# Performance work log

Hardware: AMD Instinct MI355X
Metric: run time of the kernel (lower is better)

## Reference

```python
import jax, jax.numpy as jnp
import numpy as np

N, C = 8192, 64

def setup_inputs() -> dict:
    key = jax.random.key(0)
    kA, kY = jax.random.split(key)
    A = jax.random.uniform(kA, (N, N), dtype=jnp.float32)
    Y = jax.random.normal(kY, (N, C), dtype=jnp.float32)
    return {"A": A, "Y": Y}

def reference(A, Y):
    # soft assignments
    Ys = jax.nn.softmax(Y, axis=1)                 # [n, C]
    # M[i, j] = Y_i^T A Y_j  (C x C); diag == total_ewc, strict-upper == pairwise ice
    M = jnp.einsum('ni,nm,mj->ij', Ys, A, Ys)      # two GEMMs, no n x n x C tensor
    total_ewc = jnp.diag(M)                        # [C]
    nwc = Ys.sum(axis=0)                           # [C]
    max_ewc = (nwc * (nwc - 1.0) + 1e-08) / 2.0
    cohesion = (total_ewc / max_ewc).sum()
    inter_cluster_edges = jnp.sum(jnp.triu(M, 1))  # sum_{i<j} Y_i^T A Y_j
    total_edges = A.sum()
    coupling = inter_cluster_edges / (total_edges + 1e-09)
    return -cohesion + coupling
```

## Files before the change

### kernel.cpp

```cpp
#include <hip/hip_runtime.h>
#include <hip/hip_bf16.h>

#define NN 8192
#define CC 64
#define KSPLIT 8
#define KCHUNK (NN / KSPLIT)
#define BK 64
#define NSTEPS (KCHUNK / BK)

typedef __bf16 bf16;
typedef __bf16 bf16x8 __attribute__((ext_vector_type(8)));
typedef float f32x4 __attribute__((ext_vector_type(4)));
typedef unsigned short us8 __attribute__((ext_vector_type(8)));

__global__ __launch_bounds__(256) void k1_softmax(const float* __restrict__ Yin,
                                                  float* __restrict__ Ys,
                                                  unsigned short* __restrict__ YsT,
                                                  float* __restrict__ nwc_part) {
    __shared__ float lds_t[64][65];
    __shared__ float nwc_lds[4][64];
    const int t = threadIdx.x;
    const int w = t >> 6, lane = t & 63;
    const int b = blockIdx.x;
    const int r0 = b * 64;
    float nwc_acc = 0.f;
    for (int it = 0; it < 16; ++it) {
        const int rl = it * 4 + w;
        const int row = r0 + rl;
        float y = Yin[row * CC + lane];
        float mx = y;
        #pragma unroll
        for (int m = 32; m >= 1; m >>= 1) mx = fmaxf(mx, __shfl_xor(mx, m, 64));
        float e = __expf(y - mx);
        float s = e;
        #pragma unroll
        for (int m = 32; m >= 1; m >>= 1) s += __shfl_xor(s, m, 64);
        float ys = e / s;
        Ys[row * CC + lane] = ys;
        lds_t[lane][rl] = ys;
        nwc_acc += ys;
    }
    nwc_lds[w][lane] = nwc_acc;
    __syncthreads();
    if (t < 64)
        nwc_part[b * 64 + t] = nwc_lds[0][t] + nwc_lds[1][t] + nwc_lds[2][t] + nwc_lds[3][t];
    const int c = t >> 2, q = t & 3;
    unsigned short tmp[16];
    #pragma unroll
    for (int i = 0; i < 16; ++i) {
        float v = lds_t[c][q * 16 + i];
        tmp[i] = __builtin_bit_cast(unsigned short, (__bf16)v);
    }
    us8* dst = (us8*)(&YsT[(size_t)c * NN + r0 + q * 16]);
    dst[0] = *(us8*)(&tmp[0]);
    dst[1] = *(us8*)(&tmp[8]);
}

__global__ __launch_bounds__(256) void k2_gemm(const float* __restrict__ A,
                                               const unsigned short* __restrict__ YsT,
                                               float* __restrict__ Bpart,
                                               float* __restrict__ edges_part) {
    __shared__ __align__(16) float ldsA[64 * 64];
    __shared__ __align__(16) unsigned short ldsB[64 * 64];
    __shared__ float ered[4];
    const int t = threadIdx.x;
    const int w = t >> 6, lane = t & 63;
    const int rb = blockIdx.x;
    const int kb = blockIdx.y;
    const int row0 = rb * 64;
    const int k0 = kb * KCHUNK;
    const int lq = lane >> 4;
    const int l15 = lane & 15;

    const int ar  = lane >> 4;
    const int ach = lane & 15;
    const int bc  = lane >> 3;
    const int bch = lane & 7;

    float esum = 0.f;
    f32x4 acc[4] = {};

    for (int s = 0; s < NSTEPS; ++s) {
        const int kbase = k0 + s * BK;
        __syncthreads();
        #pragma unroll
        for (int p = 0; p < 16; ++p) {
            const int r = p * 4 + ar;
            const float* src = A + (size_t)(row0 + r) * NN + kbase + ((ach ^ (r & 7)) << 2);
            __builtin_amdgcn_global_load_lds(
                (const __attribute__((address_space(1))) unsigned int*)src,
                (__attribute__((address_space(3))) unsigned int*)&ldsA[p * 256], 16, 0, 0);
        }
        #pragma unroll
        for (int q = 0; q < 8; ++q) {
            const int c = q * 8 + bc;
            const unsigned short* src = YsT + (size_t)c * NN + kbase + ((bch ^ (c & 7)) << 3);
            __builtin_amdgcn_global_load_lds(
                (const __attribute__((address_space(1))) unsigned int*)src,
                (__attribute__((address_space(3))) unsigned int*)&ldsB[q * 512], 16, 0, 0);
        }
        __syncthreads();
        #pragma unroll
        for (int kk = 0; kk < 2; ++kk) {
            const int r = w * 16 + l15;
            const int cc = kk * 8 + lq * 2;
            const int ch0 = cc ^ (r & 7);
            const f32x4 fa0 = *(const f32x4*)&ldsA[r * 64 + (ch0 << 2)];
            const f32x4 fa1 = *(const f32x4*)&ldsA[r * 64 + ((ch0 ^ 1) << 2)];
            esum += (fa0[0] + fa0[1] + fa0[2] + fa0[3]) + (fa1[0] + fa1[1] + fa1[2] + fa1[3]);
            bf16x8 a;
            a[0] = (__bf16)fa0[0]; a[1] = (__bf16)fa0[1]; a[2] = (__bf16)fa0[2]; a[3] = (__bf16)fa0[3];
            a[4] = (__bf16)fa1[0]; a[5] = (__bf16)fa1[1]; a[6] = (__bf16)fa1[2]; a[7] = (__bf16)fa1[3];
            #pragma unroll
            for (int t4 = 0; t4 < 4; ++t4) {
                const int col = t4 * 16 + l15;
                const int chB = (kk * 4 + lq) ^ (col & 7);
                const bf16x8 bb = *(const bf16x8*)&ldsB[col * 64 + (chB << 3)];
                acc[t4] = __builtin_amdgcn_mfma_f32_16x16x32_bf16(a, bb, acc[t4], 0, 0, 0);
            }
        }
    }

    const size_t base = ((size_t)kb * NN + row0) * CC;
    #pragma unroll
    for (int t4 = 0; t4 < 4; ++t4) {
        const int col = t4 * 16 + l15;
        #pragma unroll
        for (int r = 0; r < 4; ++r) {
            const int grow = w * 16 + lq * 4 + r;
            Bpart[base + (size_t)grow * CC + col] = acc[t4][r];
        }
    }
    #pragma unroll
    for (int m = 32; m >= 1; m >>= 1) esum += __shfl_xor(esum, m, 64);
    if (lane == 0) ered[w] = esum;
    __syncthreads();
    if (t == 0) edges_part[rb * KSPLIT + kb] = ered[0] + ered[1] + ered[2] + ered[3];
}

__global__ __launch_bounds__(256) void k3_mpart(const float* __restrict__ Bpart,
                                                const float* __restrict__ Ys,
                                                float* __restrict__ Mpart) {
    __shared__ float bl[4096];
    __shared__ float yl[4096];
    const int t = threadIdx.x;
    const int b = blockIdx.x;
    const int r0 = b * 64;
    for (int k = 0; k < 16; ++k) {
        const int e = k * 256 + t;
        const int i = e >> 6, c = e & 63;
        const size_t off = ((size_t)(r0 + i)) * CC + c;
        float s = 0.f;
        #pragma unroll
        for (int p = 0; p < KSPLIT; ++p) s += Bpart[(size_t)p * NN * CC + off];
        bl[e] = s;
        yl[e] = Ys[off];
    }
    __syncthreads();
    const int w = t >> 6, lane = t & 63;
    float acc[16];
    #pragma unroll
    for (int k = 0; k < 16; ++k) acc[k] = 0.f;
    for (int i = 0; i < 64; ++i) {
        const float bv = bl[i * 64 + lane];
        #pragma unroll
        for (int k = 0; k < 16; ++k)
            acc[k] += yl[i * 64 + 4 * k + w] * bv;
    }
    #pragma unroll
    for (int k = 0; k < 16; ++k)
        Mpart[(size_t)b * 4096 + k * 256 + t] = acc[k];
}

__global__ __launch_bounds__(256) void k4_reduce(const float* __restrict__ Mpart,
                                                 float* __restrict__ M) {
    const int e = blockIdx.x * 256 + threadIdx.x;
    float s = 0.f;
    for (int b = 0; b < 128; ++b) s += Mpart[(size_t)b * 4096 + e];
    M[e] = s;
}

__global__ __launch_bounds__(256) void k5_final(const float* __restrict__ M,
                                                const float* __restrict__ nwc_part,
                                                const float* __restrict__ edges_part,
                                                float* __restrict__ out) {
    __shared__ float red[256];
    const int t = threadIdx.x;
    float se = 0.f, st = 0.f, sc = 0.f;
    for (int i = t; i < 128 * KSPLIT; i += 256) se += edges_part[i];
    for (int e = t; e < 4096; e += 256) {
        const int c1 = e >> 6, c2 = e & 63;
        if (c2 > c1) st += M[e];
    }
    if (t < 64) {
        float nwc = 0.f;
        for (int b = 0; b < 128; ++b) nwc += nwc_part[b * 64 + t];
        const float me = (nwc * (nwc - 1.0f) + 1e-8f) * 0.5f;
        sc = M[t * 65] / me;
    }
    red[t] = se; __syncthreads();
    for (int s = 128; s >= 1; s >>= 1) { if (t < s) red[t] += red[t + s]; __syncthreads(); }
    const float tot_e = red[0]; __syncthreads();
    red[t] = st; __syncthreads();
    for (int s = 128; s >= 1; s >>= 1) { if (t < s) red[t] += red[t + s]; __syncthreads(); }
    const float tot_triu = red[0]; __syncthreads();
    red[t] = sc; __syncthreads();
    for (int s = 128; s >= 1; s >>= 1) { if (t < s) red[t] += red[t + s]; __syncthreads(); }
    const float cohesion = red[0];
    if (t == 0)
        out[0] = -cohesion + tot_triu / (tot_e + 1e-9f);
}

extern "C" void kernel_launch(void* const* d_in, const int* in_sizes, int n_in,
                              void* d_out, int out_size, void* d_ws, size_t ws_size,
                              hipStream_t stream) {
    const float* A   = (const float*)d_in[0];
    const float* Yin = (const float*)d_in[1];
    float* out = (float*)d_out;
    char* ws = (char*)d_ws;
    float*          Ys         = (float*)(ws + 0);
    unsigned short* YsT        = (unsigned short*)(ws + 2097152);
    float*          nwc_part   = (float*)(ws + 3145728);
    float*          edges_part = (float*)(ws + 3178496);
    float*          Bpart      = (float*)(ws + 4194304);
    float*          Mpart      = (float*)(ws + 20971520);
    float*          M          = (float*)(ws + 23068672);

    k1_softmax<<<128, 256, 0, stream>>>(Yin, Ys, YsT, nwc_part);
    k2_gemm<<<dim3(128, KSPLIT), 256, 0, stream>>>(A, YsT, Bpart, edges_part);
    k3_mpart<<<128, 256, 0, stream>>>(Bpart, Ys, Mpart);
    k4_reduce<<<16, 256, 0, stream>>>(Mpart, M);
    k5_final<<<1, 256, 0, stream>>>(M, nwc_part, edges_part, out);
}
```

Before: 132.4 us.

## Double-buffer GEMM LDS tiles and split the M-partial kernel across more blocks

The GEMM kernel now uses two LDS buffers, prefetching the next K-step's A and Ys tiles via global_load_lds while MFMAs run on the current tile. Each wave issues only its share of the loads, and there is one barrier per step. The M-partial kernel is split into 512 blocks (32 rows, half the K-splits each) for more parallelism, so the final reduction now sums 512 partials instead of 128. The trade-offs are twice the LDS per GEMM block, which may cut occupancy, and extra partial-reduction traffic.

```diff
diff --git a/kernel.cpp b/kernel.cpp
--- a/kernel.cpp
+++ b/kernel.cpp
@@ -60,8 +60,8 @@
                                                const unsigned short* __restrict__ YsT,
                                                float* __restrict__ Bpart,
                                                float* __restrict__ edges_part) {
-    __shared__ __align__(16) float ldsA[64 * 64];
-    __shared__ __align__(16) unsigned short ldsB[64 * 64];
+    __shared__ __align__(16) float ldsA[2][4096];
+    __shared__ __align__(16) unsigned short ldsB[2][4096];
     __shared__ float ered[4];
     const int t = threadIdx.x;
     const int w = t >> 6, lane = t & 63;
@@ -80,33 +80,42 @@
     float esum = 0.f;
     f32x4 acc[4] = {};
 
+    #define STAGE(buf, s)                                                                     \
+    {                                                                                         \
+        const int kbase_ = k0 + (s) * BK;                                                     \
+        _Pragma("unroll")                                                                     \
+        for (int i_ = 0; i_ < 4; ++i_) {                                                      \
+            const int p_ = w * 4 + i_;                                                        \
+            const int r_ = p_ * 4 + ar;                                                       \
+            const float* src_ = A + (size_t)(row0 + r_) * NN + kbase_ + ((ach ^ (r_ & 7)) << 2); \
+            __builtin_amdgcn_global_load_lds(                                                 \
+                (const __attribute__((address_space(1))) unsigned int*)src_,                  \
+                (__attribute__((address_space(3))) unsigned int*)&ldsA[buf][p_ * 256], 16, 0, 0); \
+        }                                                                                     \
+        _Pragma("unroll")                                                                     \
+        for (int j_ = 0; j_ < 2; ++j_) {                                                      \
+            const int q_ = w * 2 + j_;                                                        \
+            const int c_ = q_ * 8 + bc;                                                       \
+            const unsigned short* srcb_ = YsT + (size_t)c_ * NN + kbase_ + ((bch ^ (c_ & 7)) << 3); \
+            __builtin_amdgcn_global_load_lds(                                                 \
+                (const __attribute__((address_space(1))) unsigned int*)srcb_,                 \
+                (__attribute__((address_space(3))) unsigned int*)&ldsB[buf][q_ * 512], 16, 0, 0); \
+        }                                                                                     \
+    }
+
+    STAGE(0, 0);
+    __syncthreads();
+    int cur = 0;
+
     for (int s = 0; s < NSTEPS; ++s) {
-        const int kbase = k0 + s * BK;
-        __syncthreads();
-        #pragma unroll
-        for (int p = 0; p < 16; ++p) {
-            const int r = p * 4 + ar;
-            const float* src = A + (size_t)(row0 + r) * NN + kbase + ((ach ^ (r & 7)) << 2);
-            __builtin_amdgcn_global_load_lds(
-                (const __attribute__((address_space(1))) unsigned int*)src,
-                (__attribute__((address_space(3))) unsigned int*)&ldsA[p * 256], 16, 0, 0);
-        }
-        #pragma unroll
-        for (int q = 0; q < 8; ++q) {
-            const int c = q * 8 + bc;
-            const unsigned short* src = YsT + (size_t)c * NN + kbase + ((bch ^ (c & 7)) << 3);
-            __builtin_amdgcn_global_load_lds(
-                (const __attribute__((address_space(1))) unsigned int*)src,
-                (__attribute__((address_space(3))) unsigned int*)&ldsB[q * 512], 16, 0, 0);
-        }
-        __syncthreads();
+        if (s + 1 < NSTEPS) STAGE(cur ^ 1, s + 1);
         #pragma unroll
         for (int kk = 0; kk < 2; ++kk) {
             const int r = w * 16 + l15;
             const int cc = kk * 8 + lq * 2;
             const int ch0 = cc ^ (r & 7);
-            const f32x4 fa0 = *(const f32x4*)&ldsA[r * 64 + (ch0 << 2)];
-            const f32x4 fa1 = *(const f32x4*)&ldsA[r * 64 + ((ch0 ^ 1) << 2)];
+            const f32x4 fa0 = *(const f32x4*)&ldsA[cur][r * 64 + (ch0 << 2)];
+            const f32x4 fa1 = *(const f32x4*)&ldsA[cur][r * 64 + ((ch0 ^ 1) << 2)];
             esum += (fa0[0] + fa0[1] + fa0[2] + fa0[3]) + (fa1[0] + fa1[1] + fa1[2] + fa1[3]);
             bf16x8 a;
             a[0] = (__bf16)fa0[0]; a[1] = (__bf16)fa0[1]; a[2] = (__bf16)fa0[2]; a[3] = (__bf16)fa0[3];
@@ -115,11 +124,14 @@
             for (int t4 = 0; t4 < 4; ++t4) {
                 const int col = t4 * 16 + l15;
                 const int chB = (kk * 4 + lq) ^ (col & 7);
-                const bf16x8 bb = *(const bf16x8*)&ldsB[col * 64 + (chB << 3)];
+                const bf16x8 bb = *(const bf16x8*)&ldsB[cur][col * 64 + (chB << 3)];
                 acc[t4] = __builtin_amdgcn_mfma_f32_16x16x32_bf16(a, bb, acc[t4], 0, 0, 0);
             }
         }
-    }
+        __syncthreads();
+        cur ^= 1;
+    }
+    #undef STAGE
 
     const size_t base = ((size_t)kb * NN + row0) * CC;
     #pragma unroll
@@ -141,18 +153,19 @@
 __global__ __launch_bounds__(256) void k3_mpart(const float* __restrict__ Bpart,
                                                 const float* __restrict__ Ys,
                                                 float* __restrict__ Mpart) {
-    __shared__ float bl[4096];
-    __shared__ float yl[4096];
+    __shared__ float bl[2048];
+    __shared__ float yl[2048];
     const int t = threadIdx.x;
     const int b = blockIdx.x;
-    const int r0 = b * 64;
-    for (int k = 0; k < 16; ++k) {
+    const int ph = blockIdx.y;
+    const int r0 = b * 32;
+    for (int k = 0; k < 8; ++k) {
         const int e = k * 256 + t;
         const int i = e >> 6, c = e & 63;
         const size_t off = ((size_t)(r0 + i)) * CC + c;
         float s = 0.f;
         #pragma unroll
-        for (int p = 0; p < KSPLIT; ++p) s += Bpart[(size_t)p * NN * CC + off];
+        for (int j = 0; j < 4; ++j) s += Bpart[(size_t)(ph * 4 + j) * NN * CC + off];
         bl[e] = s;
         yl[e] = Ys[off];
     }
@@ -161,7 +174,7 @@
     float acc[16];
     #pragma unroll
     for (int k = 0; k < 16; ++k) acc[k] = 0.f;
-    for (int i = 0; i < 64; ++i) {
+    for (int i = 0; i < 32; ++i) {
         const float bv = bl[i * 64 + lane];
         #pragma unroll
         for (int k = 0; k < 16; ++k)
@@ -169,14 +182,14 @@
     }
     #pragma unroll
     for (int k = 0; k < 16; ++k)
-        Mpart[(size_t)b * 4096 + k * 256 + t] = acc[k];
+        Mpart[(size_t)(b * 2 + ph) * 4096 + k * 256 + t] = acc[k];
 }
 
 __global__ __launch_bounds__(256) void k4_reduce(const float* __restrict__ Mpart,
                                                  float* __restrict__ M) {
     const int e = blockIdx.x * 256 + threadIdx.x;
     float s = 0.f;
-    for (int b = 0; b < 128; ++b) s += Mpart[(size_t)b * 4096 + e];
+    for (int b = 0; b < 512; ++b) s += Mpart[(size_t)b * 4096 + e];
     M[e] = s;
 }
 
@@ -224,11 +237,11 @@
     float*          edges_part = (float*)(ws + 3178496);
     float*          Bpart      = (float*)(ws + 4194304);
     float*          Mpart      = (float*)(ws + 20971520);
-    float*          M          = (float*)(ws + 23068672);
+    float*          M          = (float*)(ws + 29360128);
 
     k1_softmax<<<128, 256, 0, stream>>>(Yin, Ys, YsT, nwc_part);
     k2_gemm<<<dim3(128, KSPLIT), 256, 0, stream>>>(A, YsT, Bpart, edges_part);
-    k3_mpart<<<128, 256, 0, stream>>>(Bpart, Ys, Mpart);
+    k3_mpart<<<dim3(256, 2), 256, 0, stream>>>(Bpart, Ys, Mpart);
     k4_reduce<<<16, 256, 0, stream>>>(Mpart, M);
     k5_final<<<1, 256, 0, stream>>>(M, nwc_part, edges_part, out);
 }
```

New measurement: 131.1 us. About the same (-1.0%).

## Split K across waves in GEMM with per-wave double-buffered A and register-held Ys

Applied to the files above, without the earlier changes.

Each GEMM block now covers 16 rows of A. Its four waves each take their own quarter of the K range, with a private double-buffered LDS slice for A. The bf16 Ys^T fragments are read directly from global memory into registers, and the per-iteration block barriers are gone. The K split drops from 8 to 2, and partial products are summed across waves in LDS before one store per block. This shrinks the partial-B buffer that k3 must write and reread. The risks are more global traffic for Ys^T and reliance on the compiler placing the right wait counts around the async LDS loads.

```diff
diff --git a/kernel.cpp b/kernel.cpp
--- a/kernel.cpp
+++ b/kernel.cpp
@@ -3,10 +3,11 @@
 
 #define NN 8192
 #define CC 64
-#define KSPLIT 8
-#define KCHUNK (NN / KSPLIT)
+#define KSPLIT 2
+#define KHALF (NN / KSPLIT)
+#define KWAVE (KHALF / 4)
 #define BK 64
-#define NSTEPS (KCHUNK / BK)
+#define WSTEPS (KWAVE / BK)
 
 typedef __bf16 bf16;
 typedef __bf16 bf16x8 __attribute__((ext_vector_type(8)));
@@ -60,82 +61,90 @@
                                                const unsigned short* __restrict__ YsT,
                                                float* __restrict__ Bpart,
                                                float* __restrict__ edges_part) {
-    __shared__ __align__(16) float ldsA[64 * 64];
-    __shared__ __align__(16) unsigned short ldsB[64 * 64];
+    __shared__ __align__(16) char shraw[32768];
     __shared__ float ered[4];
     const int t = threadIdx.x;
     const int w = t >> 6, lane = t & 63;
     const int rb = blockIdx.x;
     const int kb = blockIdx.y;
-    const int row0 = rb * 64;
-    const int k0 = kb * KCHUNK;
+    const int row0 = rb * 16;
+    const int k0w = kb * KHALF + w * KWAVE;
     const int lq = lane >> 4;
     const int l15 = lane & 15;
 
-    const int ar  = lane >> 4;
-    const int ach = lane & 15;
-    const int bc  = lane >> 3;
-    const int bch = lane & 7;
+    float* ldsA = (float*)shraw + w * 2048;
 
     float esum = 0.f;
     f32x4 acc[4] = {};
 
-    for (int s = 0; s < NSTEPS; ++s) {
-        const int kbase = k0 + s * BK;
-        __syncthreads();
-        #pragma unroll
-        for (int p = 0; p < 16; ++p) {
-            const int r = p * 4 + ar;
-            const float* src = A + (size_t)(row0 + r) * NN + kbase + ((ach ^ (r & 7)) << 2);
-            __builtin_amdgcn_global_load_lds(
-                (const __attribute__((address_space(1))) unsigned int*)src,
-                (__attribute__((address_space(3))) unsigned int*)&ldsA[p * 256], 16, 0, 0);
+    #define STAGEW(buf, kpos)                                                                  \
+    {                                                                                          \
+        _Pragma("unroll")                                                                      \
+        for (int p_ = 0; p_ < 4; ++p_) {                                                       \
+            const int r_ = p_ * 4 + lq;                                                        \
+            const int c4_ = (l15 ^ r_) & 15;                                                   \
+            const float* src_ = A + (size_t)(row0 + r_) * NN + (kpos) + c4_ * 4;               \
+            __builtin_amdgcn_global_load_lds(                                                  \
+                (const __attribute__((address_space(1))) unsigned int*)src_,                   \
+                (__attribute__((address_space(3))) unsigned int*)(ldsA + (buf) * 1024 + p_ * 256), \
+                16, 0, 0);                                                                     \
+        }                                                                                      \
+    }
+
+    STAGEW(0, k0w);
+    int cur = 0;
+    for (int s = 0; s < WSTEPS; ++s) {
+        if (s + 1 < WSTEPS) STAGEW(cur ^ 1, k0w + (s + 1) * BK);
+        bf16x8 bf0[4], bf1[4];
+        #pragma unroll
+        for (int t4 = 0; t4 < 4; ++t4) {
+            const unsigned short* pb = YsT + (size_t)(t4 * 16 + l15) * NN + k0w + s * BK + lq * 8;
+            bf0[t4] = *(const bf16x8*)(pb);
+            bf1[t4] = *(const bf16x8*)(pb + 32);
         }
         #pragma unroll
-        for (int q = 0; q < 8; ++q) {
-            const int c = q * 8 + bc;
-            const unsigned short* src = YsT + (size_t)c * NN + kbase + ((bch ^ (c & 7)) << 3);
-            __builtin_amdgcn_global_load_lds(
-                (const __attribute__((address_space(1))) unsigned int*)src,
-                (__attribute__((address_space(3))) unsigned int*)&ldsB[q * 512], 16, 0, 0);
-        }
-        __syncthreads();
-        #pragma unroll
         for (int kk = 0; kk < 2; ++kk) {
-            const int r = w * 16 + l15;
-            const int cc = kk * 8 + lq * 2;
-            const int ch0 = cc ^ (r & 7);
-            const f32x4 fa0 = *(const f32x4*)&ldsA[r * 64 + (ch0 << 2)];
-            const f32x4 fa1 = *(const f32x4*)&ldsA[r * 64 + ((ch0 ^ 1) << 2)];
+            const int e = kk * 8 + lq * 2;
+            const f32x4 fa0 = *(const f32x4*)(ldsA + cur * 1024 + l15 * 64 + ((e ^ l15) & 15) * 4);
+            const f32x4 fa1 = *(const f32x4*)(ldsA + cur * 1024 + l15 * 64 + (((e + 1) ^ l15) & 15) * 4);
             esum += (fa0[0] + fa0[1] + fa0[2] + fa0[3]) + (fa1[0] + fa1[1] + fa1[2] + fa1[3]);
             bf16x8 a;
             a[0] = (__bf16)fa0[0]; a[1] = (__bf16)fa0[1]; a[2] = (__bf16)fa0[2]; a[3] = (__bf16)fa0[3];
             a[4] = (__bf16)fa1[0]; a[5] = (__bf16)fa1[1]; a[6] = (__bf16)fa1[2]; a[7] = (__bf16)fa1[3];
-            #pragma unroll
-            for (int t4 = 0; t4 < 4; ++t4) {
-                const int col = t4 * 16 + l15;
-                const int chB = (kk * 4 + lq) ^ (col & 7);
-                const bf16x8 bb = *(const bf16x8*)&ldsB[col * 64 + (chB << 3)];
-                acc[t4] = __builtin_amdgcn_mfma_f32_16x16x32_bf16(a, bb, acc[t4], 0, 0, 0);
+            if (kk == 0) {
+                #pragma unroll
+                for (int t4 = 0; t4 < 4; ++t4)
+                    acc[t4] = __builtin_amdgcn_mfma_f32_16x16x32_bf16(a, bf0[t4], acc[t4], 0, 0, 0);
+            } else {
+                #pragma unroll
+                for (int t4 = 0; t4 < 4; ++t4)
+                    acc[t4] = __builtin_amdgcn_mfma_f32_16x16x32_bf16(a, bf1[t4], acc[t4], 0, 0, 0);
             }
         }
-    }
-
-    const size_t base = ((size_t)kb * NN + row0) * CC;
-    #pragma unroll
-    for (int t4 = 0; t4 < 4; ++t4) {
-        const int col = t4 * 16 + l15;
-        #pragma unroll
-        for (int r = 0; r < 4; ++r) {
-            const int grow = w * 16 + lq * 4 + r;
-            Bpart[base + (size_t)grow * CC + col] = acc[t4][r];
-        }
-    }
+        cur ^= 1;
+    }
+    #undef STAGEW
+
+    __syncthreads();
+    float (*bsum)[16][64] = (float(*)[16][64])shraw;
+    #pragma unroll
+    for (int t4 = 0; t4 < 4; ++t4)
+        #pragma unroll
+        for (int r = 0; r < 4; ++r)
+            bsum[w][lq * 4 + r][t4 * 16 + l15] = acc[t4][r];
     #pragma unroll
     for (int m = 32; m >= 1; m >>= 1) esum += __shfl_xor(esum, m, 64);
     if (lane == 0) ered[w] = esum;
     __syncthreads();
-    if (t == 0) edges_part[rb * KSPLIT + kb] = ered[0] + ered[1] + ered[2] + ered[3];
+    const size_t base = (size_t)kb * NN * CC + (size_t)row0 * CC;
+    #pragma unroll
+    for (int i = 0; i < 4; ++i) {
+        const int e = i * 256 + t;
+        const int row = e >> 6, col = e & 63;
+        const float sv = bsum[0][row][col] + bsum[1][row][col] + bsum[2][row][col] + bsum[3][row][col];
+        Bpart[base + (size_t)row * CC + col] = sv;
+    }
+    if (t == 0) edges_part[blockIdx.y * 512 + rb] = ered[0] + ered[1] + ered[2] + ered[3];
 }
 
 __global__ __launch_bounds__(256) void k3_mpart(const float* __restrict__ Bpart,
@@ -187,7 +196,7 @@
     __shared__ float red[256];
     const int t = threadIdx.x;
     float se = 0.f, st = 0.f, sc = 0.f;
-    for (int i = t; i < 128 * KSPLIT; i += 256) se += edges_part[i];
+    for (int i = t; i < 1024; i += 256) se += edges_part[i];
     for (int e = t; e < 4096; e += 256) {
         const int c1 = e >> 6, c2 = e & 63;
         if (c2 > c1) st += M[e];
@@ -223,11 +232,11 @@
     float*          nwc_part   = (float*)(ws + 3145728);
     float*          edges_part = (float*)(ws + 3178496);
     float*          Bpart      = (float*)(ws + 4194304);
-    float*          Mpart      = (float*)(ws + 20971520);
-    float*          M          = (float*)(ws + 23068672);
+    float*          Mpart      = (float*)(ws + 12582912);
+    float*          M          = (float*)(ws + 14680064);
 
     k1_softmax<<<128, 256, 0, stream>>>(Yin, Ys, YsT, nwc_part);
-    k2_gemm<<<dim3(128, KSPLIT), 256, 0, stream>>>(A, YsT, Bpart, edges_part);
+    k2_gemm<<<dim3(512, KSPLIT), 256, 0, stream>>>(A, YsT, Bpart, edges_part);
     k3_mpart<<<128, 256, 0, stream>>>(Bpart, Ys, Mpart);
     k4_reduce<<<16, 256, 0, stream>>>(Mpart, M);
     k5_final<<<1, 256, 0, stream>>>(M, nwc_part, edges_part, out);
```

Measured after the change: 118.6 us. 10.4% less time.
